# Kernel tuning notes

Measured on AMD Instinct MI355X. Metric: run time of the kernel, lower is better.

The kernel has to match this reference:

```python
import jax, jax.numpy as jnp
import numpy as np

B, T, D = 1, 2048, 2048
H, HD = 16, 128          # n_heads, head_dim
RD = 64                  # rotary_emb_dim
K = 4                    # short conv kernel size
EPS = 1e-5


def setup_inputs() -> dict:
    key = jax.random.key(0)
    ks = jax.random.split(key, 10)
    hidden_states = jax.random.normal(ks[0], (B, T, D), dtype=jnp.float32)
    # standard RoPE tables for the rotary sub-dimension
    inv_freq = 1.0 / (10000.0 ** (jnp.arange(0, RD, 2, dtype=jnp.float32) / RD))  # [RD/2]
    pos = jnp.arange(T, dtype=jnp.float32)
    freqs = pos[:, None] * inv_freq[None, :]          # [T, RD/2]
    emb = jnp.concatenate([freqs, freqs], axis=-1)    # [T, RD]
    cos = jnp.broadcast_to(jnp.cos(emb)[None], (B, T, RD))
    sin = jnp.broadcast_to(jnp.sin(emb)[None], (B, T, RD))
    s = 1.0 / np.sqrt(D)
    return {
        "hidden_states": hidden_states,
        "cos": cos, "sin": sin,
        "Wq": jax.random.normal(ks[1], (D, D), jnp.float32) * s,
        "Wk": jax.random.normal(ks[2], (D, D), jnp.float32) * s,
        "Wv": jax.random.normal(ks[3], (D, D), jnp.float32) * s,
        "Wo": jax.random.normal(ks[4], (D, D), jnp.float32) * s,
        "conv_q_w": jax.random.normal(ks[5], (D, K), jnp.float32) * 0.5,
        "conv_k_w": jax.random.normal(ks[6], (D, K), jnp.float32) * 0.5,
        "conv_v_w": jax.random.normal(ks[7], (D, K), jnp.float32) * 0.5,
        "q_norm_w": jnp.ones((HD,), jnp.float32),
        "k_norm_w": jnp.ones((HD,), jnp.float32),
    }


def _causal_conv_silu(x, w):
    # x: [B,T,D], w: [D,K]; depthwise causal conv (tap K-1 hits current pos) + SiLU
    xp = jnp.pad(x, ((0, 0), (K - 1, 0), (0, 0)))
    y = sum(xp[:, j:j + T, :] * w[None, None, :, j] for j in range(K))
    return jax.nn.silu(y)


def _rms_norm(x, w):
    # x: [..., HD]
    var = jnp.mean(x * x, axis=-1, keepdims=True)
    return x * jax.lax.rsqrt(var + EPS) * w


def _rotate_half(x):
    x1, x2 = x[..., : x.shape[-1] // 2], x[..., x.shape[-1] // 2:]
    return jnp.concatenate([-x2, x1], axis=-1)


def _apply_rope(x, cos, sin):
    # x: [B,H,T,HD]; cos/sin: [B,T,RD] -> unsqueeze head dim; partial rotary branch
    cos = cos[:, None, :, :]
    sin = sin[:, None, :, :]
    x_rot, x_pass = x[..., :RD], x[..., RD:]
    x_rot = x_rot * cos + _rotate_half(x_rot) * sin
    # faithful to source: negates rotated part when rotary_dim != head_dim
    return jnp.concatenate([-x_rot, x_pass], axis=-1)


def reference(hidden_states, cos, sin, Wq, Wk, Wv, Wo,
              conv_q_w, conv_k_w, conv_v_w, q_norm_w, k_norm_w):
    # projections (Linear with bias=False: y = x @ W^T)
    q = hidden_states @ Wq.T
    k = hidden_states @ Wk.T
    v = hidden_states @ Wv.T
    # short causal depthwise conv + SiLU
    q = _causal_conv_silu(q, conv_q_w)
    k = _causal_conv_silu(k, conv_k_w)
    v = _causal_conv_silu(v, conv_v_w)
    # split heads: [B,T,D] -> [B,T,H,HD]
    q = q.reshape(B, T, H, HD)
    k = k.reshape(B, T, H, HD)
    v = v.reshape(B, T, H, HD)
    # per-head RMSNorm, then [B,H,T,HD]
    q = _rms_norm(q, q_norm_w).transpose(0, 2, 1, 3)
    k = _rms_norm(k, k_norm_w).transpose(0, 2, 1, 3)
    v = v.transpose(0, 2, 1, 3)
    # RoPE (partial)
    q = _apply_rope(q, cos, sin)
    k = _apply_rope(k, cos, sin)
    # causal attention
    scale = 1.0 / np.sqrt(HD)
    scores = jnp.einsum('bhqd,bhkd->bhqk', q, k) * scale
    causal = jnp.tril(jnp.ones((T, T), dtype=bool))
    scores = jnp.where(causal[None, None], scores, jnp.float32(-1e30))
    probs = jax.nn.softmax(scores, axis=-1)
    attn = jnp.einsum('bhqk,bhkd->bhqd', probs, v)
    # [B,H,T,HD] -> [B,T,D], output projection
    out = attn.transpose(0, 2, 1, 3).reshape(B, T, D) @ Wo.T
    return out
```

## Files before the change

### kernel.cpp

```cpp
#include <hip/hip_runtime.h>
#include <hip/hip_bf16.h>

#define T_SEQ 2048
#define D_MODEL 2048
#define NH 16
#define HDIM 128
#define RD_ROT 64

typedef __bf16 bf16x8 __attribute__((ext_vector_type(8)));
typedef float f32x4 __attribute__((ext_vector_type(4)));

__device__ __forceinline__ void async_copy16(const __bf16* g, __bf16* l) {
    __builtin_amdgcn_global_load_lds(
        (const __attribute__((address_space(1))) void*)g,
        (__attribute__((address_space(3))) void*)l, 16, 0, 0);
}

__global__ __launch_bounds__(256) void cast_kernel(
    const float* __restrict__ s0, const float* __restrict__ s1, const float* __restrict__ s2,
    const float* __restrict__ s3, const float* __restrict__ s4,
    __bf16* __restrict__ d0, __bf16* __restrict__ d1, __bf16* __restrict__ d2,
    __bf16* __restrict__ d3, __bf16* __restrict__ d4)
{
    const float* s; __bf16* d;
    switch (blockIdx.y) {
        case 0: s = s0; d = d0; break;
        case 1: s = s1; d = d1; break;
        case 2: s = s2; d = d2; break;
        case 3: s = s3; d = d3; break;
        default: s = s4; d = d4; break;
    }
    size_t base = (size_t)blockIdx.x * D_MODEL + (size_t)threadIdx.x * 8;
    f32x4 a = *(const f32x4*)(s + base);
    f32x4 b = *(const f32x4*)(s + base + 4);
    bf16x8 o;
    #pragma unroll
    for (int i = 0; i < 4; i++) { o[i] = (__bf16)a[i]; o[i + 4] = (__bf16)b[i]; }
    *(bf16x8*)(d + base) = o;
}

__global__ __launch_bounds__(256) void gemm_bt_kernel(
    const __bf16* __restrict__ A,
    const __bf16* __restrict__ B0, const __bf16* __restrict__ B1, const __bf16* __restrict__ B2,
    __bf16* __restrict__ C0, __bf16* __restrict__ C1, __bf16* __restrict__ C2)
{
    constexpr int BM = 128, BK = 32, KD = D_MODEL, NIT = KD / BK;
    const __bf16* Bm = blockIdx.z == 0 ? B0 : (blockIdx.z == 1 ? B1 : B2);
    __bf16* Cm       = blockIdx.z == 0 ? C0 : (blockIdx.z == 1 ? C1 : C2);

    __shared__ __align__(16) __bf16 As[2][BM * BK];
    __shared__ __align__(16) __bf16 Bs[2][BM * BK];

    const int lane = threadIdx.x & 63;
    const int wave = threadIdx.x >> 6;
    const int r15  = lane & 15;
    const int quad = lane >> 4;
    const int bm = blockIdx.x * BM;
    const int bn = blockIdx.y * BM;
    const int wm = (wave >> 1) * 64;
    const int wn = (wave & 1) * 64;

    f32x4 acc[4][4] = {};

    const int srow = wave * 32 + (lane >> 2);
    const int sg   = (lane & 3) ^ ((lane >> 2) & 3);

    const __bf16* Arow0 = A  + (size_t)(bm + srow)      * KD + sg * 8;
    const __bf16* Arow1 = A  + (size_t)(bm + srow + 16) * KD + sg * 8;
    const __bf16* Brow0 = Bm + (size_t)(bn + srow)      * KD + sg * 8;
    const __bf16* Brow1 = Bm + (size_t)(bn + srow + 16) * KD + sg * 8;

    async_copy16(Arow0, &As[0][wave * 1024]);
    async_copy16(Arow1, &As[0][wave * 1024 + 512]);
    async_copy16(Brow0, &Bs[0][wave * 1024]);
    async_copy16(Brow1, &Bs[0][wave * 1024 + 512]);

    for (int it = 0; it < NIT; it++) {
        const int buf = it & 1;
        __syncthreads();

        if (it + 1 < NIT) {
            const int k0 = (it + 1) * BK;
            const int nb = buf ^ 1;
            async_copy16(Arow0 + k0, &As[nb][wave * 1024]);
            async_copy16(Arow1 + k0, &As[nb][wave * 1024 + 512]);
            async_copy16(Brow0 + k0, &Bs[nb][wave * 1024]);
            async_copy16(Brow1 + k0, &Bs[nb][wave * 1024 + 512]);
        }

        bf16x8 av[4], bv[4];
        #pragma unroll
        for (int mt = 0; mt < 4; mt++)
            av[mt] = *(const bf16x8*)&As[buf][(wm + mt * 16 + r15) * BK + ((quad ^ (r15 & 3)) << 3)];
        #pragma unroll
        for (int nt = 0; nt < 4; nt++)
            bv[nt] = *(const bf16x8*)&Bs[buf][(wn + nt * 16 + r15) * BK + ((quad ^ (r15 & 3)) << 3)];
        #pragma unroll
        for (int mt = 0; mt < 4; mt++)
            #pragma unroll
            for (int nt = 0; nt < 4; nt++)
                acc[mt][nt] = __builtin_amdgcn_mfma_f32_16x16x32_bf16(av[mt], bv[nt], acc[mt][nt], 0, 0, 0);
    }

    #pragma unroll
    for (int mt = 0; mt < 4; mt++) {
        #pragma unroll
        for (int r = 0; r < 4; r++) {
            size_t row = bm + wm + mt * 16 + quad * 4 + r;
            #pragma unroll
            for (int nt = 0; nt < 4; nt++) {
                size_t col = bn + wn + nt * 16 + r15;
                Cm[row * D_MODEL + col] = (__bf16)acc[mt][nt][r];
            }
        }
    }
}

__global__ __launch_bounds__(256) void gemm_bt_splitk_kernel(
    const __bf16* __restrict__ A, const __bf16* __restrict__ Bm, float* __restrict__ C)
{
    constexpr int BM = 128, BK = 32, KD = D_MODEL, NIT = (KD / 2) / BK;
    __shared__ __align__(16) __bf16 As[2][BM * BK];
    __shared__ __align__(16) __bf16 Bs[2][BM * BK];

    const int lane = threadIdx.x & 63;
    const int wave = threadIdx.x >> 6;
    const int r15  = lane & 15;
    const int quad = lane >> 4;
    const int bm = blockIdx.x * BM;
    const int bn = blockIdx.y * BM;
    const int wm = (wave >> 1) * 64;
    const int wn = (wave & 1) * 64;
    const int kbase = blockIdx.z * (KD / 2);

    f32x4 acc[4][4] = {};
    const int srow = wave * 32 + (lane >> 2);
    const int sg   = (lane & 3) ^ ((lane >> 2) & 3);

    const __bf16* Arow0 = A  + (size_t)(bm + srow)      * KD + kbase + sg * 8;
    const __bf16* Arow1 = A  + (size_t)(bm + srow + 16) * KD + kbase + sg * 8;
    const __bf16* Brow0 = Bm + (size_t)(bn + srow)      * KD + kbase + sg * 8;
    const __bf16* Brow1 = Bm + (size_t)(bn + srow + 16) * KD + kbase + sg * 8;

    async_copy16(Arow0, &As[0][wave * 1024]);
    async_copy16(Arow1, &As[0][wave * 1024 + 512]);
    async_copy16(Brow0, &Bs[0][wave * 1024]);
    async_copy16(Brow1, &Bs[0][wave * 1024 + 512]);

    for (int it = 0; it < NIT; it++) {
        const int buf = it & 1;
        __syncthreads();

        if (it + 1 < NIT) {
            const int k0 = (it + 1) * BK;
            const int nb = buf ^ 1;
            async_copy16(Arow0 + k0, &As[nb][wave * 1024]);
            async_copy16(Arow1 + k0, &As[nb][wave * 1024 + 512]);
            async_copy16(Brow0 + k0, &Bs[nb][wave * 1024]);
            async_copy16(Brow1 + k0, &Bs[nb][wave * 1024 + 512]);
        }

        bf16x8 av[4], bv[4];
        #pragma unroll
        for (int mt = 0; mt < 4; mt++)
            av[mt] = *(const bf16x8*)&As[buf][(wm + mt * 16 + r15) * BK + ((quad ^ (r15 & 3)) << 3)];
        #pragma unroll
        for (int nt = 0; nt < 4; nt++)
            bv[nt] = *(const bf16x8*)&Bs[buf][(wn + nt * 16 + r15) * BK + ((quad ^ (r15 & 3)) << 3)];
        #pragma unroll
        for (int mt = 0; mt < 4; mt++)
            #pragma unroll
            for (int nt = 0; nt < 4; nt++)
                acc[mt][nt] = __builtin_amdgcn_mfma_f32_16x16x32_bf16(av[mt], bv[nt], acc[mt][nt], 0, 0, 0);
    }

    #pragma unroll
    for (int mt = 0; mt < 4; mt++) {
        #pragma unroll
        for (int r = 0; r < 4; r++) {
            size_t row = bm + wm + mt * 16 + quad * 4 + r;
            #pragma unroll
            for (int nt = 0; nt < 4; nt++) {
                size_t col = bn + wn + nt * 16 + r15;
                atomicAdd(&C[row * D_MODEL + col], acc[mt][nt][r]);
            }
        }
    }
}

__global__ __launch_bounds__(256) void preproc_qk_kernel(
    const __bf16* __restrict__ q_raw, const __bf16* __restrict__ k_raw,
    const float* __restrict__ cwq, const float* __restrict__ cwk,
    const float* __restrict__ qnw, const float* __restrict__ knw,
    const float* __restrict__ cosb, const float* __restrict__ sinb,
    __bf16* __restrict__ q_proc, __bf16* __restrict__ k_proc)
{
    const int t = blockIdx.x;
    const int which = blockIdx.y;
    const __bf16* X = which ? k_raw : q_raw;
    const float*  W = which ? cwk : cwq;
    const float*  nw = which ? knw : qnw;
    __bf16* P = which ? k_proc : q_proc;
    const float SC = which ? 1.0f : 0.08838834764831845f;

    const int tid = threadIdx.x;
    const int c0  = tid * 8;
    const int h   = tid >> 4;
    const int dl0 = (tid & 15) * 8;

    f32x4 wv[8];
    #pragma unroll
    for (int i = 0; i < 8; i++) wv[i] = *(const f32x4*)&W[(c0 + i) * 4];

    float acc[8] = {};
    #pragma unroll
    for (int j = 0; j < 4; j++) {
        int tt = t + j - 3;
        if (tt >= 0) {
            bf16x8 xv = *(const bf16x8*)&X[(size_t)tt * D_MODEL + c0];
            #pragma unroll
            for (int i = 0; i < 8; i++) acc[i] += (float)xv[i] * wv[i][j];
        }
    }
    float sil[8], ss = 0.f;
    #pragma unroll
    for (int i = 0; i < 8; i++) {
        float s = acc[i] / (1.f + __expf(-acc[i]));
        sil[i] = s; ss += s * s;
    }
    #pragma unroll
    for (int off = 1; off < 16; off <<= 1) ss += __shfl_xor(ss, off);
    float inv = rsqrtf(ss * (1.f / 128.f) + 1e-5f);

    f32x4 nv0 = *(const f32x4*)&nw[dl0];
    f32x4 nv1 = *(const f32x4*)&nw[dl0 + 4];
    float yn[8];
    #pragma unroll
    for (int i = 0; i < 8; i++) yn[i] = sil[i] * inv * (i < 4 ? nv0[i] : nv1[i - 4]);

    float partner[8];
    #pragma unroll
    for (int i = 0; i < 8; i++) partner[i] = __shfl_xor(yn[i], 4);

    bf16x8 o;
    if (dl0 < RD_ROT) {
        f32x4 cv0 = *(const f32x4*)&cosb[t * RD_ROT + dl0];
        f32x4 cv1 = *(const f32x4*)&cosb[t * RD_ROT + dl0 + 4];
        f32x4 sv0 = *(const f32x4*)&sinb[t * RD_ROT + dl0];
        f32x4 sv1 = *(const f32x4*)&sinb[t * RD_ROT + dl0 + 4];
        #pragma unroll
        for (int i = 0; i < 8; i++) {
            int dl = dl0 + i;
            float c = i < 4 ? cv0[i] : cv1[i - 4];
            float s = i < 4 ? sv0[i] : sv1[i - 4];
            float rot = (dl < 32) ? -partner[i] : partner[i];
            o[i] = (__bf16)((yn[i] * c + rot * s) * SC);
        }
    } else {
        #pragma unroll
        for (int i = 0; i < 8; i++) o[i] = (__bf16)(yn[i] * SC);
    }
    *(bf16x8*)&P[((size_t)h * T_SEQ + t) * HDIM + dl0] = o;
}

__global__ __launch_bounds__(128) void preproc_v_kernel(
    const __bf16* __restrict__ v_raw, const float* __restrict__ cwv,
    __bf16* __restrict__ v_t)
{
    const int t0 = blockIdx.x * 8;
    const int h = blockIdx.y;
    const int dl = threadIdx.x;
    const int d = h * HDIM + dl;

    f32x4 wv = *(const f32x4*)&cwv[d * 4];
    float x[11];
    #pragma unroll
    for (int m = 0; m < 11; m++) {
        int tt = t0 - 3 + m;
        x[m] = (tt >= 0) ? (float)v_raw[(size_t)tt * D_MODEL + d] : 0.f;
    }
    bf16x8 o;
    #pragma unroll
    for (int r = 0; r < 8; r++) {
        float y = x[r] * wv[0] + x[r + 1] * wv[1] + x[r + 2] * wv[2] + x[r + 3] * wv[3];
        o[r] = (__bf16)(y / (1.f + __expf(-y)));
    }
    *(bf16x8*)&v_t[((size_t)h * HDIM + dl) * T_SEQ + t0] = o;
}

__global__ __launch_bounds__(256, 2) void attn_kernel(
    const __bf16* __restrict__ Qp,
    const __bf16* __restrict__ Kp,
    const __bf16* __restrict__ Vt,
    __bf16* __restrict__ Op)
{
    constexpr int TK = 64, PSTR = 72;
    __shared__ __align__(16) __bf16 Ks[2][TK * HDIM];
    __shared__ __align__(16) __bf16 Vs[2][HDIM * TK];
    __shared__ __align__(16) __bf16 Ps[64 * PSTR];

    const int lane = threadIdx.x & 63;
    const int wave = threadIdx.x >> 6;
    const int r15  = lane & 15;
    const int quad = lane >> 4;
    const int h = blockIdx.y;
    const int qi = (blockIdx.y & 8) ? ((int)gridDim.x - 1 - (int)blockIdx.x) : (int)blockIdx.x;
    const int q0 = qi * TK;

    const __bf16* Kb = Kp + (size_t)h * T_SEQ * HDIM;
    const __bf16* Vb = Vt + (size_t)h * HDIM * T_SEQ;

    const int kchunk = wave * 4;
    const int krow_l = (lane >> 4);
    const int kg     = lane & 15;
    const int vrow_l = (lane >> 3);
    const int vg     = lane & 7;

    bf16x8 qf[4];
    const __bf16* qbase = Qp + ((size_t)h * T_SEQ + q0 + wave * 16 + r15) * HDIM;
    #pragma unroll
    for (int s = 0; s < 4; s++) qf[s] = *(const bf16x8*)(qbase + s * 32 + quad * 8);

    f32x4 oacc[8] = {};
    float lsum[4] = {};

    const int ntk = qi + 1;

    #pragma unroll
    for (int i = 0; i < 4; i++) {
        int ck = kchunk + i;
        int krow = ck * 4 + krow_l;
        int vrow = ck * 8 + vrow_l;
        async_copy16(Kb + (size_t)krow * HDIM + (kg ^ (krow & 15)) * 8, &Ks[0][ck * 512]);
        async_copy16(Vb + (size_t)vrow * T_SEQ + (vg ^ (vrow & 7)) * 8, &Vs[0][ck * 512]);
    }

    for (int it = 0; it < ntk; it++) {
        const int buf = it & 1;
        const bool last = (it == ntk - 1);
        __syncthreads();

        if (!last) {
            const int tkn = (it + 1) * TK;
            const int nbuf = buf ^ 1;
            #pragma unroll
            for (int i = 0; i < 4; i++) {
                int ck = kchunk + i;
                int krow = ck * 4 + krow_l;
                int vrow = ck * 8 + vrow_l;
                async_copy16(Kb + (size_t)(tkn + krow) * HDIM + (kg ^ (krow & 15)) * 8, &Ks[nbuf][ck * 512]);
                async_copy16(Vb + (size_t)vrow * T_SEQ + tkn + (vg ^ (vrow & 7)) * 8, &Vs[nbuf][ck * 512]);
            }
        }

        f32x4 sacc[4] = {};
        #pragma unroll
        for (int s = 0; s < 4; s++) {
            #pragma unroll
            for (int nt = 0; nt < 4; nt++) {
                bf16x8 kf = *(const bf16x8*)&Ks[buf][(nt * 16 + r15) * HDIM + (((s * 4 + quad) ^ r15) << 3)];
                sacc[nt] = __builtin_amdgcn_mfma_f32_16x16x32_bf16(qf[s], kf, sacc[nt], 0, 0, 0);
            }
        }

        #pragma unroll
        for (int nt = 0; nt < 4; nt++) {
            #pragma unroll
            for (int r = 0; r < 4; r++) {
                float p = __expf(sacc[nt][r]);
                if (last) {
                    int qrow = q0 + wave * 16 + quad * 4 + r;
                    int kcol = it * TK + nt * 16 + r15;
                    if (kcol > qrow) p = 0.f;
                }
                sacc[nt][r] = p;
                lsum[r] += p;
            }
        }

        #pragma unroll
        for (int nt = 0; nt < 4; nt++)
            #pragma unroll
            for (int r = 0; r < 4; r++)
                Ps[(wave * 16 + quad * 4 + r) * PSTR + nt * 16 + r15] = (__bf16)sacc[nt][r];

        #pragma unroll
        for (int s2 = 0; s2 < 2; s2++) {
            bf16x8 pf = *(const bf16x8*)&Ps[(wave * 16 + r15) * PSTR + s2 * 32 + quad * 8];
            #pragma unroll
            for (int nt = 0; nt < 8; nt++) {
                bf16x8 vf = *(const bf16x8*)&Vs[buf][(nt * 16 + r15) * TK + (((s2 * 4 + quad) ^ (r15 & 7)) << 3)];
                oacc[nt] = __builtin_amdgcn_mfma_f32_16x16x32_bf16(pf, vf, oacc[nt], 0, 0, 0);
            }
        }
    }

    #pragma unroll
    for (int r = 0; r < 4; r++) {
        float l = lsum[r];
        #pragma unroll
        for (int off = 1; off < 16; off <<= 1) l += __shfl_xor(l, off);
        float inv = 1.0f / l;
        size_t row = q0 + wave * 16 + quad * 4 + r;
        #pragma unroll
        for (int nt = 0; nt < 8; nt++)
            Op[row * D_MODEL + h * HDIM + nt * 16 + r15] = (__bf16)(oacc[nt][r] * inv);
    }
}

extern "C" void kernel_launch(void* const* d_in, const int* in_sizes, int n_in,
                              void* d_out, int out_size, void* d_ws, size_t ws_size,
                              hipStream_t stream) {
    (void)in_sizes; (void)n_in; (void)out_size; (void)ws_size;
    const float* hidden = (const float*)d_in[0];
    const float* cosb   = (const float*)d_in[1];
    const float* sinb   = (const float*)d_in[2];
    const float* Wq     = (const float*)d_in[3];
    const float* Wk     = (const float*)d_in[4];
    const float* Wv     = (const float*)d_in[5];
    const float* Wo     = (const float*)d_in[6];
    const float* cwq    = (const float*)d_in[7];
    const float* cwk    = (const float*)d_in[8];
    const float* cwv    = (const float*)d_in[9];
    const float* qnw    = (const float*)d_in[10];
    const float* knw    = (const float*)d_in[11];

    const size_t NEL = (size_t)T_SEQ * D_MODEL;
    __bf16* ws = (__bf16*)d_ws;
    __bf16* h_bf   = ws + 0 * NEL;
    __bf16* Wq_bf  = ws + 1 * NEL;
    __bf16* Wk_bf  = ws + 2 * NEL;
    __bf16* Wv_bf  = ws + 3 * NEL;
    __bf16* Wo_bf  = ws + 4 * NEL;
    __bf16* q_raw  = ws + 5 * NEL;
    __bf16* k_raw  = ws + 6 * NEL;
    __bf16* v_raw  = ws + 7 * NEL;
    __bf16* q_proc = Wq_bf;
    __bf16* k_proc = Wk_bf;
    __bf16* v_t    = Wv_bf;
    __bf16* attn_b = h_bf;
    float*  out    = (float*)d_out;

    cast_kernel<<<dim3(T_SEQ, 5), 256, 0, stream>>>(hidden, Wq, Wk, Wv, Wo,
                                                    h_bf, Wq_bf, Wk_bf, Wv_bf, Wo_bf);
    gemm_bt_kernel<<<dim3(16, 16, 3), 256, 0, stream>>>(
        h_bf, Wq_bf, Wk_bf, Wv_bf, q_raw, k_raw, v_raw);
    preproc_qk_kernel<<<dim3(T_SEQ, 2), 256, 0, stream>>>(
        q_raw, k_raw, cwq, cwk, qnw, knw, cosb, sinb, q_proc, k_proc);
    preproc_v_kernel<<<dim3(T_SEQ / 8, NH), 128, 0, stream>>>(v_raw, cwv, v_t);
    attn_kernel<<<dim3(T_SEQ / 64, NH), 256, 0, stream>>>(q_proc, k_proc, v_t, attn_b);
    hipMemsetAsync(d_out, 0, NEL * sizeof(float), stream);
    gemm_bt_splitk_kernel<<<dim3(16, 16, 2), 256, 0, stream>>>(attn_b, Wo_bf, out);
}
```

Measured before the change: 343.3 us.

## Rewrite QKV projection GEMM as 256x256 tile, 8-wave, phased ping-pong pipeline

Replaces the 128x128/BK=32 QKV GEMM with a 256x256 tile, BK=64, 512-thread kernel. Each K step is split into four MFMA phases separated by barriers, with prefetch two tiles ahead and priority raising during MFMA. It also adds an XOR-swizzled LDS layout and a swizzled block order for L2 locality. The aim is more operand reuse and better overlap of global loads with MFMA, at the cost of more registers, more LDS (128KB per block), and only 192 blocks.

```diff
diff --git a/kernel.cpp b/kernel.cpp
--- a/kernel.cpp
+++ b/kernel.cpp
@@ -39,78 +39,164 @@
     *(bf16x8*)(d + base) = o;
 }
 
-__global__ __launch_bounds__(256) void gemm_bt_kernel(
+__device__ __forceinline__ bf16x8 ld_frag(const __bf16* lds, int rr, int s, int quad, int r7) {
+    return *(const bf16x8*)&lds[rr * 64 + ((((s << 2) + quad) ^ r7) << 3)];
+}
+
+__global__ __launch_bounds__(512, 2) void gemm_qkv_8ph_kernel(
     const __bf16* __restrict__ A,
     const __bf16* __restrict__ B0, const __bf16* __restrict__ B1, const __bf16* __restrict__ B2,
     __bf16* __restrict__ C0, __bf16* __restrict__ C1, __bf16* __restrict__ C2)
 {
-    constexpr int BM = 128, BK = 32, KD = D_MODEL, NIT = KD / BK;
-    const __bf16* Bm = blockIdx.z == 0 ? B0 : (blockIdx.z == 1 ? B1 : B2);
-    __bf16* Cm       = blockIdx.z == 0 ? C0 : (blockIdx.z == 1 ? C1 : C2);
+    constexpr int BM = 256, BK = 64, KD = D_MODEL, NT = KD / BK;
 
     __shared__ __align__(16) __bf16 As[2][BM * BK];
     __shared__ __align__(16) __bf16 Bs[2][BM * BK];
 
-    const int lane = threadIdx.x & 63;
-    const int wave = threadIdx.x >> 6;
+    const int flat = (int)blockIdx.x + 8 * ((int)blockIdx.y + 8 * (int)blockIdx.z);
+    const int swz  = (flat & 7) * 24 + (flat >> 3);
+    const int bz   = swz >> 6;
+    const int bm   = (swz & 7) * BM;
+    const int bn   = ((swz >> 3) & 7) * BM;
+
+    const __bf16* Bmat = bz == 0 ? B0 : (bz == 1 ? B1 : B2);
+    __bf16* Cmat       = bz == 0 ? C0 : (bz == 1 ? C1 : C2);
+
+    const int tid  = threadIdx.x;
+    const int lane = tid & 63;
+    const int wave = tid >> 6;
     const int r15  = lane & 15;
     const int quad = lane >> 4;
-    const int bm = blockIdx.x * BM;
-    const int bn = blockIdx.y * BM;
-    const int wm = (wave >> 1) * 64;
-    const int wn = (wave & 1) * 64;
-
-    f32x4 acc[4][4] = {};
-
-    const int srow = wave * 32 + (lane >> 2);
-    const int sg   = (lane & 3) ^ ((lane >> 2) & 3);
-
-    const __bf16* Arow0 = A  + (size_t)(bm + srow)      * KD + sg * 8;
-    const __bf16* Arow1 = A  + (size_t)(bm + srow + 16) * KD + sg * 8;
-    const __bf16* Brow0 = Bm + (size_t)(bn + srow)      * KD + sg * 8;
-    const __bf16* Brow1 = Bm + (size_t)(bn + srow + 16) * KD + sg * 8;
-
-    async_copy16(Arow0, &As[0][wave * 1024]);
-    async_copy16(Arow1, &As[0][wave * 1024 + 512]);
-    async_copy16(Brow0, &Bs[0][wave * 1024]);
-    async_copy16(Brow1, &Bs[0][wave * 1024 + 512]);
-
-    for (int it = 0; it < NIT; it++) {
-        const int buf = it & 1;
-        __syncthreads();
-
-        if (it + 1 < NIT) {
-            const int k0 = (it + 1) * BK;
-            const int nb = buf ^ 1;
-            async_copy16(Arow0 + k0, &As[nb][wave * 1024]);
-            async_copy16(Arow1 + k0, &As[nb][wave * 1024 + 512]);
-            async_copy16(Brow0 + k0, &Bs[nb][wave * 1024]);
-            async_copy16(Brow1 + k0, &Bs[nb][wave * 1024 + 512]);
-        }
-
-        bf16x8 av[4], bv[4];
-        #pragma unroll
-        for (int mt = 0; mt < 4; mt++)
-            av[mt] = *(const bf16x8*)&As[buf][(wm + mt * 16 + r15) * BK + ((quad ^ (r15 & 3)) << 3)];
-        #pragma unroll
-        for (int nt = 0; nt < 4; nt++)
-            bv[nt] = *(const bf16x8*)&Bs[buf][(wn + nt * 16 + r15) * BK + ((quad ^ (r15 & 3)) << 3)];
-        #pragma unroll
-        for (int mt = 0; mt < 4; mt++)
-            #pragma unroll
-            for (int nt = 0; nt < 4; nt++)
-                acc[mt][nt] = __builtin_amdgcn_mfma_f32_16x16x32_bf16(av[mt], bv[nt], acc[mt][nt], 0, 0, 0);
-    }
-
-    #pragma unroll
-    for (int mt = 0; mt < 4; mt++) {
+    const int r7   = r15 & 7;
+    const int wm   = wave >> 2;
+    const int wn   = wave & 3;
+
+    const int sr8 = lane >> 3;
+    const int sck = (lane & 7) ^ sr8;
+    const __bf16* Ap = A    + (size_t)(bm + wave * 16 + sr8) * KD + sck * 8;
+    const __bf16* Bp = Bmat + (size_t)(bn + wave * 16 + sr8) * KD + sck * 8;
+
+    auto stageA = [&](int buf, int h, int kt) {
+        const __bf16* s = Ap + (size_t)(h * 128) * KD + kt;
+        __bf16* d = &As[buf][h * 8192 + wave * 1024];
+        async_copy16(s, d);
+        async_copy16(s + 8 * KD, d + 512);
+    };
+    auto stageB = [&](int buf, int h, int kt) {
+        const __bf16* s = Bp + (size_t)(h * 128) * KD + kt;
+        __bf16* d = &Bs[buf][h * 8192 + wave * 1024];
+        async_copy16(s, d);
+        async_copy16(s + 8 * KD, d + 512);
+    };
+
+    f32x4 acc[8][4] = {};
+
+    stageA(0, 0, 0);  stageA(0, 1, 0);  stageB(0, 0, 0);  stageB(0, 1, 0);
+    stageA(1, 0, BK); stageA(1, 1, BK); stageB(1, 0, BK); stageB(1, 1, BK);
+    asm volatile("s_waitcnt vmcnt(8)" ::: "memory");
+    __builtin_amdgcn_s_barrier();
+
+    for (int t = 0; t < NT; t++) {
+        const int b = t & 1;
+        const __bf16* Asb = As[b];
+        const __bf16* Bsb = Bs[b];
+        const bool pf = (t + 2 < NT);
+        const int ktp = (t + 2) * BK;
+
+        bf16x8 a0[4][2], a1[4][2], b0[2][2], b1[2][2];
+
+        #pragma unroll
+        for (int mf = 0; mf < 4; mf++)
+            #pragma unroll
+            for (int s = 0; s < 2; s++)
+                a0[mf][s] = ld_frag(Asb, wm * 128 + mf * 16 + r15, s, quad, r7);
+        #pragma unroll
+        for (int nf = 0; nf < 2; nf++)
+            #pragma unroll
+            for (int s = 0; s < 2; s++)
+                b0[nf][s] = ld_frag(Bsb, wn * 64 + nf * 16 + r15, s, quad, r7);
+        __builtin_amdgcn_s_barrier();
+        asm volatile("s_waitcnt lgkmcnt(0)" ::: "memory");
+        __builtin_amdgcn_sched_barrier(0);
+        __builtin_amdgcn_s_setprio(1);
+        #pragma unroll
+        for (int mf = 0; mf < 4; mf++)
+            #pragma unroll
+            for (int nf = 0; nf < 2; nf++)
+                #pragma unroll
+                for (int s = 0; s < 2; s++)
+                    acc[mf][nf] = __builtin_amdgcn_mfma_f32_16x16x32_bf16(a0[mf][s], b0[nf][s], acc[mf][nf], 0, 0, 0);
+        __builtin_amdgcn_s_setprio(0);
+        __builtin_amdgcn_sched_barrier(0);
+        __builtin_amdgcn_s_barrier();
+
+        #pragma unroll
+        for (int mf = 0; mf < 4; mf++)
+            #pragma unroll
+            for (int s = 0; s < 2; s++)
+                a1[mf][s] = ld_frag(Asb, wm * 128 + 64 + mf * 16 + r15, s, quad, r7);
+        #pragma unroll
+        for (int nf = 0; nf < 2; nf++)
+            #pragma unroll
+            for (int s = 0; s < 2; s++)
+                b1[nf][s] = ld_frag(Bsb, wn * 64 + 32 + nf * 16 + r15, s, quad, r7);
+        __builtin_amdgcn_s_barrier();
+        asm volatile("s_waitcnt lgkmcnt(0)" ::: "memory");
+        __builtin_amdgcn_sched_barrier(0);
+        __builtin_amdgcn_s_setprio(1);
+        #pragma unroll
+        for (int mf = 0; mf < 4; mf++)
+            #pragma unroll
+            for (int nf = 0; nf < 2; nf++)
+                #pragma unroll
+                for (int s = 0; s < 2; s++)
+                    acc[4 + mf][2 + nf] = __builtin_amdgcn_mfma_f32_16x16x32_bf16(a1[mf][s], b1[nf][s], acc[4 + mf][2 + nf], 0, 0, 0);
+        __builtin_amdgcn_s_setprio(0);
+        __builtin_amdgcn_sched_barrier(0);
+        __builtin_amdgcn_s_barrier();
+
+        if (pf) { stageA(b, 0, ktp); stageB(b, 0, ktp); }
+        __builtin_amdgcn_s_barrier();
+        __builtin_amdgcn_s_setprio(1);
+        #pragma unroll
+        for (int mf = 0; mf < 4; mf++)
+            #pragma unroll
+            for (int nf = 0; nf < 2; nf++)
+                #pragma unroll
+                for (int s = 0; s < 2; s++)
+                    acc[mf][2 + nf] = __builtin_amdgcn_mfma_f32_16x16x32_bf16(a0[mf][s], b1[nf][s], acc[mf][2 + nf], 0, 0, 0);
+        __builtin_amdgcn_s_setprio(0);
+        __builtin_amdgcn_sched_barrier(0);
+        __builtin_amdgcn_s_barrier();
+
+        if (pf) { stageA(b, 1, ktp); stageB(b, 1, ktp); }
+        __builtin_amdgcn_s_barrier();
+        __builtin_amdgcn_s_setprio(1);
+        #pragma unroll
+        for (int mf = 0; mf < 4; mf++)
+            #pragma unroll
+            for (int nf = 0; nf < 2; nf++)
+                #pragma unroll
+                for (int s = 0; s < 2; s++)
+                    acc[4 + mf][nf] = __builtin_amdgcn_mfma_f32_16x16x32_bf16(a1[mf][s], b0[nf][s], acc[4 + mf][nf], 0, 0, 0);
+        __builtin_amdgcn_s_setprio(0);
+        __builtin_amdgcn_sched_barrier(0);
+        if (t + 1 < NT) {
+            if (pf) asm volatile("s_waitcnt vmcnt(8)" ::: "memory");
+            else    asm volatile("s_waitcnt vmcnt(0)" ::: "memory");
+        }
+        __builtin_amdgcn_s_barrier();
+    }
+
+    #pragma unroll
+    for (int mf = 0; mf < 8; mf++) {
         #pragma unroll
         for (int r = 0; r < 4; r++) {
-            size_t row = bm + wm + mt * 16 + quad * 4 + r;
-            #pragma unroll
-            for (int nt = 0; nt < 4; nt++) {
-                size_t col = bn + wn + nt * 16 + r15;
-                Cm[row * D_MODEL + col] = (__bf16)acc[mt][nt][r];
+            const size_t row = (size_t)(bm + wm * 128 + mf * 16 + quad * 4 + r);
+            #pragma unroll
+            for (int nf = 0; nf < 4; nf++) {
+                const size_t col = (size_t)(bn + wn * 64 + nf * 16 + r15);
+                Cmat[row * D_MODEL + col] = (__bf16)acc[mf][nf][r];
             }
         }
     }
@@ -443,7 +529,7 @@
 
     cast_kernel<<<dim3(T_SEQ, 5), 256, 0, stream>>>(hidden, Wq, Wk, Wv, Wo,
                                                     h_bf, Wq_bf, Wk_bf, Wv_bf, Wo_bf);
-    gemm_bt_kernel<<<dim3(16, 16, 3), 256, 0, stream>>>(
+    gemm_qkv_8ph_kernel<<<dim3(8, 8, 3), 512, 0, stream>>>(
         h_bf, Wq_bf, Wk_bf, Wv_bf, q_raw, k_raw, v_raw);
     preproc_qk_kernel<<<dim3(T_SEQ, 2), 256, 0, stream>>>(
         q_raw, k_raw, cwq, cwk, qnw, knw, cosb, sinb, q_proc, k_proc);
```

Result: no change. 340.8 us (-0.7%).
